# Kernel tuning notes

Measured on AMD Instinct MI355X. Metric: run time of the kernel, lower is better.

## Reference

```python
import jax, jax.numpy as jnp
import numpy as np

T, D, H, C, MAXLEN = 1024, 512, 512, 50257, 150


def setup_inputs() -> dict:
    key = jax.random.key(0)
    ks = iter(jax.random.split(key, 32))
    s = 0.1  # keep gates out of saturation
    def p(shape):
        return jax.random.normal(next(ks), shape, jnp.float32) * s
    return {
        "x": jax.random.normal(next(ks), (T, D), jnp.float32),
        "enc_Wih0": p((2, 4 * H, D)), "enc_Whh0": p((2, 4 * H, H)), "enc_b0": p((2, 4 * H)),
        "enc_Wih1": p((2, 4 * H, 2 * H)), "enc_Whh1": p((2, 4 * H, H)), "enc_b1": p((2, 4 * H)),
        "dec_Wih0": p((2, 4 * H, D)), "dec_Whh0": p((2, 4 * H, H)), "dec_b0": p((2, 4 * H)),
        "dec_Wih1": p((2, 4 * H, 2 * H)), "dec_Whh1": p((2, 4 * H, H)), "dec_b1": p((2, 4 * H)),
        "lin_W": p((C, 2 * H)), "lin_b": p((C,)),
        "emb": p((C, D)),
        "bos": p((D,)),
        "out_max_len": MAXLEN,
    }


def _cell(x, h, c, Wih, Whh, b):
    # PyTorch LSTM gate order: i, f, g, o; b = b_ih + b_hh
    g = Wih @ x + Whh @ h + b
    i, f, gg, o = jnp.split(g, 4)
    c = jax.nn.sigmoid(f) * c + jax.nn.sigmoid(i) * jnp.tanh(gg)
    h = jax.nn.sigmoid(o) * jnp.tanh(c)
    return h, c


def _run_dir(xs, Wih, Whh, b, reverse):
    Hh = Whh.shape[1]
    init = (jnp.zeros((Hh,), xs.dtype), jnp.zeros((Hh,), xs.dtype))
    def step(carry, xt):
        h, c = carry
        h, c = _cell(xt, h, c, Wih, Whh, b)
        return (h, c), h
    (hT, cT), hs = jax.lax.scan(step, init, xs, reverse=reverse)
    return hs, hT, cT  # hs aligned with input order


def _encode(x, layers):
    xs = x  # [T, D]
    h_fin, c_fin = [], []
    for (Wih, Whh, b) in layers:
        hs_f, hf, cf = _run_dir(xs, Wih[0], Whh[0], b[0], False)
        hs_b, hb, cb = _run_dir(xs, Wih[1], Whh[1], b[1], True)
        xs = jnp.concatenate([hs_f, hs_b], axis=-1)  # [T, 2H]
        h_fin.append(jnp.stack([hf, hb]))
        c_fin.append(jnp.stack([cf, cb]))
    return jnp.stack(h_fin), jnp.stack(c_fin)  # [L, 2, H]


def reference(x, enc_Wih0, enc_Whh0, enc_b0, enc_Wih1, enc_Whh1, enc_b1,
              dec_Wih0, dec_Whh0, dec_b0, dec_Wih1, dec_Whh1, dec_b1,
              lin_W, lin_b, emb, bos, out_max_len):
    layers_enc = [(enc_Wih0, enc_Whh0, enc_b0), (enc_Wih1, enc_Whh1, enc_b1)]
    layers_dec = [(dec_Wih0, dec_Whh0, dec_b0), (dec_Wih1, dec_Whh1, dec_b1)]

    h, c = _encode(x, layers_enc)  # [2, 2, H] each

    def dec_step(carry, _):
        buf, h, c = carry
        inp = buf
        nh, nc = [], []
        for l, (Wih, Whh, b) in enumerate(layers_dec):
            hf, cf = _cell(inp, h[l, 0], c[l, 0], Wih[0], Whh[0], b[0])
            hb, cb = _cell(inp, h[l, 1], c[l, 1], Wih[1], Whh[1], b[1])
            inp = jnp.concatenate([hf, hb])  # [2H]
            nh.append(jnp.stack([hf, hb]))
            nc.append(jnp.stack([cf, cb]))
        logits = lin_W @ inp + lin_b          # [C]
        tok = jnp.argmax(logits)              # greedy feedback
        buf = emb[tok]                        # [D]
        return (buf, jnp.stack(nh), jnp.stack(nc)), (logits, tok)

    _, (logits_seq, toks) = jax.lax.scan(dec_step, (bos, h, c), None, length=out_max_len)
    return logits_seq, toks  # [L_out, C], [L_out]
```

## Files before the change

### kernel.cpp

```cpp
#include <hip/hip_runtime.h>
#include <hip/hip_fp16.h>

typedef unsigned int u32;
typedef unsigned short u16;
typedef unsigned long long u64;

#define DEV static __device__ __forceinline__

DEV float sigf(float x){ return 1.0f / (1.0f + expf(-x)); }

DEV u64  ldA64(const u64* p){ return __hip_atomic_load(p, __ATOMIC_RELAXED, __HIP_MEMORY_SCOPE_AGENT); }
DEV void stA64(u64* p, u64 v){ __hip_atomic_store(p, v, __ATOMIC_RELAXED, __HIP_MEMORY_SCOPE_AGENT); }
DEV float ldAf(const float* p){ return __hip_atomic_load(p, __ATOMIC_RELAXED, __HIP_MEMORY_SCOPE_AGENT); }
DEV void stAf(float* p, float v){ __hip_atomic_store(p, v, __ATOMIC_RELAXED, __HIP_MEMORY_SCOPE_AGENT); }
DEV u32  ldA32(const u32* p){ return __hip_atomic_load(p, __ATOMIC_RELAXED, __HIP_MEMORY_SCOPE_AGENT); }

DEV u64 packHV(float h, u32 tag){ return (((u64)__float_as_uint(h)) << 32) | (u64)tag; }
DEV float unpackH(u64 v){ return __uint_as_float((u32)(v >> 32)); }

DEV u64 packKeyT(float v, u32 row, u32 tagv){
  u32 u = __float_as_uint(v);
  u = (u & 0x80000000u) ? ~u : (u | 0x80000000u);
  return (((u64)u) << 32) | ((u64)(0x1FFFFu - row) << 15) | (u64)tagv;
}

DEV float dot8h(const uint4 A, const float4 a, const float4 b){
  const __half2* h = (const __half2*)&A;
  const float2 f0 = __half22float2(h[0]);
  const float2 f1 = __half22float2(h[1]);
  const float2 f2 = __half22float2(h[2]);
  const float2 f3 = __half22float2(h[3]);
  float s;
  s  = f0.x*a.x + f0.y*a.y + f1.x*a.z + f1.y*a.w;
  s += f2.x*b.x + f2.y*b.y + f3.x*b.z + f3.y*b.w;
  return s;
}

DEV float dotrow(const float4 A, const float4 B, const float4 Cc, const float4 D,
                 const float4 q0, const float4 q1, const float4 q2, const float4 q3){
  float s;
  s  = A.x*q0.x + A.y*q0.y + A.z*q0.z + A.w*q0.w;
  s += B.x*q1.x + B.y*q1.y + B.z*q1.z + B.w*q1.w;
  s += Cc.x*q2.x + Cc.y*q2.y + Cc.z*q2.z + Cc.w*q2.w;
  s += D.x*q3.x + D.y*q3.y + D.z*q3.z + D.w*q3.w;
  return s;
}

struct SM {
  float w1s[24576];
  float inpP[1600];
  float linp[1024];
  float h0c[1024];
  float srow[200];
  float erow[200];
  float red[8];
  float dots[16];
  float cst0[4];
  float cst1[4];
  u64   wkey[4];
};

template<int CPT> DEV int pidx(int c){ int b = c / CPT; return b * (CPT + 4) + (c - b * CPT); }

template<int CPT, int DIN>
DEV void loadw(float* wreg, const float* Wih, const float* Whh, int jb4){
  const int tid = threadIdx.x, r = tid >> 4, p = tid & 15;
  const int R = 512 * (r >> 2) + jb4 + (r & 3);
  const float* s1 = Wih + (size_t)R * DIN;
  const float* s2 = Whh + (size_t)R * 512;
  #pragma unroll
  for (int k = 0; k < CPT; k += 4){
    const int col = p * CPT + k;
    const float4 v = *(const float4*)((col < DIN) ? (s1 + col) : (s2 + col - DIN));
    wreg[k] = v.x; wreg[k+1] = v.y; wreg[k+2] = v.z; wreg[k+3] = v.w;
  }
}

template<int CPT>
DEV void dot16(const float* wreg, const float* inpP, float* dots){
  const int tid = threadIdx.x, p = tid & 15;
  const float* xi = inpP + p * (CPT + 4);
  float acc = 0.f;
  #pragma unroll
  for (int k = 0; k < CPT; k += 4){
    const float4 xv = *(const float4*)(xi + k);
    acc = fmaf(wreg[k],   xv.x, acc);
    acc = fmaf(wreg[k+1], xv.y, acc);
    acc = fmaf(wreg[k+2], xv.z, acc);
    acc = fmaf(wreg[k+3], xv.w, acc);
  }
  #pragma unroll
  for (int s = 1; s < 16; s <<= 1) acc += __shfl_xor(acc, s, 64);
  if (p == 0) dots[tid >> 4] = acc;
}

DEV void dot16_w1(const float* w1s, const float* inpP, float* dots){
  const int tid = threadIdx.x, p = tid & 15;
  const float* xi = inpP + p * 100;
  float acc = 0.f;
  #pragma unroll
  for (int k = 0; k < 96; k += 4){
    const float4 w4 = *(const float4*)(w1s + (k >> 2) * 1024 + tid * 4);
    const float4 xv = *(const float4*)(xi + k);
    acc = fmaf(w4.x, xv.x, acc);
    acc = fmaf(w4.y, xv.y, acc);
    acc = fmaf(w4.z, xv.z, acc);
    acc = fmaf(w4.w, xv.w, acc);
  }
  #pragma unroll
  for (int s = 1; s < 16; s <<= 1) acc += __shfl_xor(acc, s, 64);
  if (p == 0) dots[tid >> 4] = acc;
}

DEV void gbar_phase(u32* g, u32 ev){
  __syncthreads();
  if (threadIdx.x == 0){
    __hip_atomic_fetch_add(g, 1u, __ATOMIC_RELEASE, __HIP_MEMORY_SCOPE_AGENT);
    const u32 tgt = 256u * ev;
    while (ldA32(g) < tgt) __builtin_amdgcn_s_sleep(8);
    (void)__hip_atomic_fetch_add(g, 0u, __ATOMIC_ACQUIRE, __HIP_MEMORY_SCOPE_AGENT);
    asm volatile("" ::: "memory");
  }
  __syncthreads();
}

template<int DIN, bool WRITE_XS>
DEV void enc_layer(const float* __restrict__ xg, float* __restrict__ xs_out,
                   const float* __restrict__ Wih, const float* __restrict__ Whh,
                   const float* __restrict__ bias,
                   u64* __restrict__ ht, float* __restrict__ hfinL, float* __restrict__ cfinL,
                   const int dir, const int jb4, SM& sm)
{
  constexpr int CPT = (DIN + 512) / 16;
  constexpr int NX  = DIN / 256;
  const int tid = threadIdx.x;
  float wreg[CPT];
  loadw<CPT, DIN>(wreg, Wih + (size_t)dir * 2048 * DIN, Whh + (size_t)dir * 2048 * 512, jb4);
  float b_i = 0.f, b_f = 0.f, b_g = 0.f, b_o = 0.f;
  if (tid < 4){
    const int j = jb4 + tid;
    sm.cst0[tid] = 0.f;
    b_i = bias[dir*2048 +        j];
    b_f = bias[dir*2048 +  512 + j];
    b_g = bias[dir*2048 + 1024 + j];
    b_o = bias[dir*2048 + 1536 + j];
  }
  float xr[NX];
  {
    const int t0 = dir ? 1023 : 0;
    #pragma unroll
    for (int i = 0; i < NX; ++i){
      const int c = tid + 256 * i;
      xr[i] = (DIN == 512) ? xg[(size_t)t0 * DIN + c] : ldAf(xg + (size_t)t0 * DIN + c);
    }
  }
  for (int step = 0; step < 1024; ++step){
    #pragma unroll
    for (int i = 0; i < NX; ++i) sm.inpP[pidx<CPT>(tid + 256 * i)] = xr[i];
    {
      const u64* hp = ht + (step & 1) * 512;
      const u32 want = (u32)step;
      u64 a = ldA64(hp + tid*2), b = ldA64(hp + tid*2 + 1);
      while ((u32)a != want){ __builtin_amdgcn_s_sleep(1); a = ldA64(hp + tid*2); }
      while ((u32)b != want){ __builtin_amdgcn_s_sleep(1); b = ldA64(hp + tid*2 + 1); }
      sm.inpP[pidx<CPT>(DIN + tid*2)]     = unpackH(a);
      sm.inpP[pidx<CPT>(DIN + tid*2 + 1)] = unpackH(b);
    }
    __syncthreads();
    if (step < 1023){
      const int tn = dir ? (1022 - step) : (step + 1);
      #pragma unroll
      for (int i = 0; i < NX; ++i){
        const int c = tid + 256 * i;
        xr[i] = (DIN == 512) ? xg[(size_t)tn * DIN + c] : ldAf(xg + (size_t)tn * DIN + c);
      }
    }
    dot16<CPT>(wreg, sm.inpP, sm.dots);
    __syncthreads();
    if (tid < 4){
      const float gi = sm.dots[tid]      + b_i;
      const float gf = sm.dots[4 + tid]  + b_f;
      const float gg = sm.dots[8 + tid]  + b_g;
      const float go = sm.dots[12 + tid] + b_o;
      const float cc = sigf(gf) * sm.cst0[tid] + sigf(gi) * tanhf(gg);
      const float hh = sigf(go) * tanhf(cc);
      sm.cst0[tid] = cc;
      const int t = dir ? (1023 - step) : step;
      const int j = jb4 + tid;
      stA64(ht + ((step + 1) & 1) * 512 + j, packHV(hh, (u32)(step + 1)));
      if (WRITE_XS) stAf(xs_out + (size_t)t * 1024 + dir * 512 + j, hh);
      if (step == 1023){ stAf(hfinL + dir*512 + j, hh); stAf(cfinL + dir*512 + j, cc); }
    }
    __syncthreads();
  }
}

__global__ void bilstm_init(u32* ws){
  for (u32 i = threadIdx.x; i < 32768u; i += 256u) ws[i] = 0u;
}

__global__ void cvt_lin(const float* __restrict__ w, uint4* __restrict__ o,
                        float* __restrict__ maxw, const int C){
  const int wv = threadIdx.x >> 6, lane = threadIdx.x & 63;
  const int stride = gridDim.x * 4;
  for (int r = blockIdx.x * 4 + wv; r < C; r += stride){
    const float4* src = (const float4*)(w + (size_t)r * 1024) + lane * 4;
    const float4 v0 = src[0], v1 = src[1], v2 = src[2], v3 = src[3];
    uint4 p0, p1;
    __half2 h;
    h = __floats2half2_rn(v0.x, v0.y); p0.x = *(const u32*)&h;
    h = __floats2half2_rn(v0.z, v0.w); p0.y = *(const u32*)&h;
    h = __floats2half2_rn(v1.x, v1.y); p0.z = *(const u32*)&h;
    h = __floats2half2_rn(v1.z, v1.w); p0.w = *(const u32*)&h;
    h = __floats2half2_rn(v2.x, v2.y); p1.x = *(const u32*)&h;
    h = __floats2half2_rn(v2.z, v2.w); p1.y = *(const u32*)&h;
    h = __floats2half2_rn(v3.x, v3.y); p1.z = *(const u32*)&h;
    h = __floats2half2_rn(v3.z, v3.w); p1.w = *(const u32*)&h;
    uint4* dst = o + (size_t)r * 128 + lane * 2;
    dst[0] = p0; dst[1] = p1;
    float m = fmaxf(fmaxf(fmaxf(fabsf(v0.x), fabsf(v0.y)), fmaxf(fabsf(v0.z), fabsf(v0.w))),
                    fmaxf(fmaxf(fabsf(v1.x), fabsf(v1.y)), fmaxf(fabsf(v1.z), fabsf(v1.w))));
    m = fmaxf(m, fmaxf(fmaxf(fabsf(v2.x), fabsf(v2.y)), fmaxf(fabsf(v2.z), fabsf(v2.w))));
    m = fmaxf(m, fmaxf(fmaxf(fabsf(v3.x), fabsf(v3.y)), fmaxf(fabsf(v3.z), fabsf(v3.w))));
    #pragma unroll
    for (int s = 1; s < 64; s <<= 1) m = fmaxf(m, __shfl_xor(m, s, 64));
    if (lane == 0) maxw[r] = m;
  }
}

template<int LINFP16>
__global__ __launch_bounds__(256, 1)
void bilstm_persist(const float* __restrict__ x,
                    const float* __restrict__ eW0, const float* __restrict__ eU0, const float* __restrict__ eb0,
                    const float* __restrict__ eW1, const float* __restrict__ eU1, const float* __restrict__ eb1,
                    const float* __restrict__ dW0, const float* __restrict__ dU0, const float* __restrict__ db0,
                    const float* __restrict__ dW1, const float* __restrict__ dU1, const float* __restrict__ db1,
                    const float* __restrict__ linW, const float* __restrict__ linb,
                    const float* __restrict__ emb, const float* __restrict__ bos,
                    float* __restrict__ out, float* __restrict__ ws, const int L, const int C)
{
  __shared__ SM sm;
  const int w = blockIdx.x;
  const int tid = threadIdx.x;
  const int dir = (w >> 2) & 1;
  const int jb4 = ((w >> 3) * 4 + (w & 3)) * 4;

  u64*  htagE = (u64*)ws;
  u64*  h0t   = htagE + 4096;
  u64*  h1t   = h0t + 2048;
  float* hfin = (float*)(h1t + 2048);
  float* cfin = hfin + 2048;
  u32*  gbar  = (u32*)(cfin + 2048);
  u64*  gkey  = (u64*)((char*)ws + 98304);
  const u16*  linH = (const u16*)((const char*)ws + 131072);
  const float* maxw = (const float*)((const char*)ws + 131072 + (size_t)C * 2048);
  float* xs1  = out;

  enc_layer<512,  true >(x,   xs1,     eW0, eU0, eb0, htagE + (0*2 + dir)*1024, hfin,        cfin,        dir, jb4, sm);
  gbar_phase(gbar, 1);
  enc_layer<1024, false>(xs1, nullptr, eW1, eU1, eb1, htagE + (1*2 + dir)*1024, hfin + 1024, cfin + 1024, dir, jb4, sm);
  gbar_phase(gbar, 2);

  float w0reg[64];
  loadw<64, 512>(w0reg, dW0 + (size_t)dir*2048*512, dU0 + (size_t)dir*2048*512, jb4);
  {
    const int r = tid >> 4, p = tid & 15;
    const int R = 512 * (r >> 2) + jb4 + (r & 3);
    const float* s1 = dW1 + (size_t)dir*2048*1024 + (size_t)R * 1024;
    const float* s2 = dU1 + (size_t)dir*2048*512  + (size_t)R * 512;
    #pragma unroll
    for (int k = 0; k < 96; k += 4){
      const int col = p * 96 + k;
      const float4 v = *(const float4*)((col < 1024) ? (s1 + col) : (s2 + col - 1024));
      *(float4*)(sm.w1s + (k >> 2) * 1024 + tid * 4) = v;
    }
  }

  float b0i=0,b0f=0,b0g=0,b0o=0, b1i=0,b1f=0,b1g=0,b1o=0;
  if (tid < 4){
    const int j = jb4 + tid;
    sm.cst0[tid] = ldAf(&cfin[dir*512 + j]);
    sm.cst1[tid] = ldAf(&cfin[1024 + dir*512 + j]);
    b0i = db0[dir*2048 + j];        b0f = db0[dir*2048 + 512 + j];
    b0g = db0[dir*2048 + 1024 + j]; b0o = db0[dir*2048 + 1536 + j];
    b1i = db1[dir*2048 + j];        b1f = db1[dir*2048 + 512 + j];
    b1g = db1[dir*2048 + 1024 + j]; b1o = db1[dir*2048 + 1536 + j];
  }
  const int rbase = w * 196 + (w < 81 ? w : 81);
  const int rn    = 196 + (w < 81 ? 1 : 0);
  int tok = 0;

  for (int t = 0; t < L; ++t){
    const u32 tag = (u32)(t + 1);
    {
      const float* src = (t == 0) ? bos : (emb + (size_t)tok * 512);
      sm.inpP[pidx<64>(tid)]       = src[tid];
      sm.inpP[pidx<64>(tid + 256)] = src[tid + 256];
      if (t == 0){
        sm.inpP[pidx<64>(512 + tid*2)]     = ldAf(&hfin[dir*512 + tid*2]);
        sm.inpP[pidx<64>(512 + tid*2 + 1)] = ldAf(&hfin[dir*512 + tid*2 + 1]);
      } else {
        sm.inpP[pidx<64>(512 + tid*2)]     = sm.h0c[dir*512 + tid*2];
        sm.inpP[pidx<64>(512 + tid*2 + 1)] = sm.h0c[dir*512 + tid*2 + 1];
      }
      __syncthreads();
      dot16<64>(w0reg, sm.inpP, sm.dots);
      __syncthreads();
      if (tid < 4){
        const float gi = sm.dots[tid] + b0i, gf = sm.dots[4+tid] + b0f;
        const float gg = sm.dots[8+tid] + b0g, go = sm.dots[12+tid] + b0o;
        const float cc = sigf(gf) * sm.cst0[tid] + sigf(gi) * tanhf(gg);
        const float hh = sigf(go) * tanhf(cc);
        sm.cst0[tid] = cc;
        stA64(h0t + (dir*2 + (t & 1))*512 + jb4 + tid, packHV(hh, tag));
      }
      __syncthreads();
    }

    {
      #pragma unroll
      for (int i = 0; i < 4; ++i){
        const int c = tid + 256 * i;
        const int d = c >> 9, idx = c & 511;
        const u64* hp = h0t + (d*2 + (t & 1)) * 512 + idx;
        u64 v = ldA64(hp);
        while ((u32)v != tag){ __builtin_amdgcn_s_sleep(1); v = ldA64(hp); }
        const float hv = unpackH(v);
        sm.inpP[pidx<96>(c)] = hv;
        sm.h0c[c] = hv;
      }
      if (t == 0){
        sm.inpP[pidx<96>(1024 + tid*2)]     = ldAf(&hfin[1024 + dir*512 + tid*2]);
        sm.inpP[pidx<96>(1024 + tid*2 + 1)] = ldAf(&hfin[1024 + dir*512 + tid*2 + 1]);
      } else {
        sm.inpP[pidx<96>(1024 + tid*2)]     = sm.linp[dir*512 + tid*2];
        sm.inpP[pidx<96>(1024 + tid*2 + 1)] = sm.linp[dir*512 + tid*2 + 1];
      }
      __syncthreads();
      dot16_w1(sm.w1s, sm.inpP, sm.dots);
      __syncthreads();
      if (tid < 4){
        const float gi = sm.dots[tid] + b1i, gf = sm.dots[4+tid] + b1f;
        const float gg = sm.dots[8+tid] + b1g, go = sm.dots[12+tid] + b1o;
        const float cc = sigf(gf) * sm.cst1[tid] + sigf(gi) * tanhf(gg);
        const float hh = sigf(go) * tanhf(cc);
        sm.cst1[tid] = cc;
        stA64(h1t + (dir*2 + (t & 1))*512 + jb4 + tid, packHV(hh, tag));
      }
    }

    {
      float pabs = 0.f;
      #pragma unroll
      for (int i = 0; i < 4; ++i){
        const int c = tid + 256 * i;
        const int d = c >> 9, idx = c & 511;
        const u64* hp = h1t + (d*2 + (t & 1)) * 512 + idx;
        u64 v = ldA64(hp);
        while ((u32)v != tag){ __builtin_amdgcn_s_sleep(1); v = ldA64(hp); }
        const float hv = unpackH(v);
        sm.linp[c] = hv;
        pabs += fabsf(hv);
      }
      const int wv = tid >> 6, lane = tid & 63;
      if constexpr (LINFP16){
        #pragma unroll
        for (int s = 1; s < 64; s <<= 1) pabs += __shfl_xor(pabs, s, 64);
        if (lane == 0) sm.red[wv] = pabs;
      }
      __syncthreads();

      const float4* ip4 = (const float4*)(sm.linp + lane * 16);
      const float4 q0 = ip4[0], q1 = ip4[1], q2 = ip4[2], q3 = ip4[3];
      u64 kmax = 0;
      const int rmaxr = rbase + rn - 1;

      if constexpr (LINFP16){
        const float sumabs = sm.red[0] + sm.red[1] + sm.red[2] + sm.red[3];
        const float cErr = sumabs * 7.5e-4f;
        float lb = -1e30f;
        for (int i0 = wv; i0 < rn; i0 += 16){
          const int ia = i0;
          const int ib = (i0 + 4  > rn - 1) ? rn - 1 : i0 + 4;
          const int ic = (i0 + 8  > rn - 1) ? rn - 1 : i0 + 8;
          const int id = (i0 + 12 > rn - 1) ? rn - 1 : i0 + 12;
          const int ra = rbase + ia, rb = rbase + ib, rc = rbase + ic, rd = rbase + id;
          const uint4* pa = (const uint4*)(linH + (size_t)ra * 1024) + lane * 2;
          const uint4* pb = (const uint4*)(linH + (size_t)rb * 1024) + lane * 2;
          const uint4* pc = (const uint4*)(linH + (size_t)rc * 1024) + lane * 2;
          const uint4* pd = (const uint4*)(linH + (size_t)rd * 1024) + lane * 2;
          const uint4 A0 = pa[0], A1 = pa[1];
          const uint4 B0 = pb[0], B1 = pb[1];
          const uint4 C0 = pc[0], C1 = pc[1];
          const uint4 D0 = pd[0], D1 = pd[1];
          float sa = dot8h(A0, q0, q1) + dot8h(A1, q2, q3);
          float sb = dot8h(B0, q0, q1) + dot8h(B1, q2, q3);
          float sc = dot8h(C0, q0, q1) + dot8h(C1, q2, q3);
          float sd = dot8h(D0, q0, q1) + dot8h(D1, q2, q3);
          #pragma unroll
          for (int sh = 1; sh < 64; sh <<= 1){
            sa += __shfl_xor(sa, sh, 64);
            sb += __shfl_xor(sb, sh, 64);
            sc += __shfl_xor(sc, sh, 64);
            sd += __shfl_xor(sd, sh, 64);
          }
          if (lane == 0){
            sa += linb[ra]; sb += linb[rb]; sc += linb[rc]; sd += linb[rd];
            out[(size_t)t * C + ra] = sa;
            out[(size_t)t * C + rb] = sb;
            out[(size_t)t * C + rc] = sc;
            out[(size_t)t * C + rd] = sd;
            const float ea = maxw[ra] * cErr + 1e-4f;
            const float eb = maxw[rb] * cErr + 1e-4f;
            const float ec = maxw[rc] * cErr + 1e-4f;
            const float ed = maxw[rd] * cErr + 1e-4f;
            sm.srow[ia] = sa; sm.erow[ia] = ea;
            sm.srow[ib] = sb; sm.erow[ib] = eb;
            sm.srow[ic] = sc; sm.erow[ic] = ec;
            sm.srow[id] = sd; sm.erow[id] = ed;
            lb = fmaxf(lb, sa - ea); lb = fmaxf(lb, sb - eb);
            lb = fmaxf(lb, sc - ec); lb = fmaxf(lb, sd - ed);
          }
        }
        if (lane == 0) sm.red[4 + wv] = lb;
        __syncthreads();
        const float Lb = fmaxf(fmaxf(sm.red[4], sm.red[5]), fmaxf(sm.red[6], sm.red[7]));
        for (int i = wv; i < rn; i += 4){
          if (sm.srow[i] + sm.erow[i] >= Lb){
            const int row = rbase + i;
            const float4* wp = (const float4*)(linW + (size_t)row * 1024) + lane * 4;
            float s = dotrow(wp[0], wp[1], wp[2], wp[3], q0, q1, q2, q3);
            #pragma unroll
            for (int sh2 = 1; sh2 < 64; sh2 <<= 1) s += __shfl_xor(s, sh2, 64);
            if (lane == 0){
              s += linb[row];
              const u64 k = packKeyT(s, (u32)row, tag);
              if (k > kmax) kmax = k;
            }
          }
        }
      } else {
        for (int i0 = wv; i0 < rn; i0 += 16){
          const int ra = rbase + i0;
          const int rb = (ra + 4  > rmaxr) ? rmaxr : ra + 4;
          const int rc = (ra + 8  > rmaxr) ? rmaxr : ra + 8;
          const int rd = (ra + 12 > rmaxr) ? rmaxr : ra + 12;
          const float ba = linb[ra], bb = linb[rb], bc = linb[rc], bd = linb[rd];
          const float4* pa = (const float4*)(linW + (size_t)ra * 1024) + lane * 4;
          const float4* pb = (const float4*)(linW + (size_t)rb * 1024) + lane * 4;
          const float4* pc = (const float4*)(linW + (size_t)rc * 1024) + lane * 4;
          const float4* pd = (const float4*)(linW + (size_t)rd * 1024) + lane * 4;
          const float4 a0 = pa[0], a1 = pa[1], a2 = pa[2], a3 = pa[3];
          const float4 e0 = pb[0], e1 = pb[1], e2 = pb[2], e3 = pb[3];
          const float4 c0 = pc[0], c1 = pc[1], c2 = pc[2], c3 = pc[3];
          const float4 d0 = pd[0], d1 = pd[1], d2 = pd[2], d3 = pd[3];
          float sa = dotrow(a0,a1,a2,a3, q0,q1,q2,q3);
          float sb = dotrow(e0,e1,e2,e3, q0,q1,q2,q3);
          float sc = dotrow(c0,c1,c2,c3, q0,q1,q2,q3);
          float sd = dotrow(d0,d1,d2,d3, q0,q1,q2,q3);
          #pragma unroll
          for (int sh = 1; sh < 64; sh <<= 1){
            sa += __shfl_xor(sa, sh, 64);
            sb += __shfl_xor(sb, sh, 64);
            sc += __shfl_xor(sc, sh, 64);
            sd += __shfl_xor(sd, sh, 64);
          }
          if (lane == 0){
            sa += ba; sb += bb; sc += bc; sd += bd;
            out[(size_t)t * C + ra] = sa;
            out[(size_t)t * C + rb] = sb;
            out[(size_t)t * C + rc] = sc;
            out[(size_t)t * C + rd] = sd;
            u64 k;
            k = packKeyT(sa, (u32)ra, tag); if (k > kmax) kmax = k;
            k = packKeyT(sb, (u32)rb, tag); if (k > kmax) kmax = k;
            k = packKeyT(sc, (u32)rc, tag); if (k > kmax) kmax = k;
            k = packKeyT(sd, (u32)rd, tag); if (k > kmax) kmax = k;
          }
        }
      }
      if (lane == 0) sm.wkey[wv] = kmax;
    }

    __syncthreads();
    if (tid == 0){
      u64 k4 = sm.wkey[0];
      if (sm.wkey[1] > k4) k4 = sm.wkey[1];
      if (sm.wkey[2] > k4) k4 = sm.wkey[2];
      if (sm.wkey[3] > k4) k4 = sm.wkey[3];
      stA64(gkey + (size_t)w * 16, k4);
    }
    __syncthreads();
    {
      const u64* p = gkey + (size_t)tid * 16;
      u64 kv = ldA64(p);
      while ((u32)(kv & 0x7FFFu) != tag){ __builtin_amdgcn_s_sleep(1); kv = ldA64(p); }
      #pragma unroll
      for (int s = 1; s < 64; s <<= 1){
        const u64 o = (u64)__shfl_xor((unsigned long long)kv, s, 64);
        if (o > kv) kv = o;
      }
      if ((tid & 63) == 0) sm.wkey[tid >> 6] = kv;
    }
    __syncthreads();
    {
      u64 gk = sm.wkey[0];
      if (sm.wkey[1] > gk) gk = sm.wkey[1];
      if (sm.wkey[2] > gk) gk = sm.wkey[2];
      if (sm.wkey[3] > gk) gk = sm.wkey[3];
      tok = (int)(0x1FFFFu - ((u32)(gk >> 15) & 0x1FFFFu));
      if (w == 0 && tid == 0) out[(size_t)L * C + t] = (float)tok;
    }
  }
}

extern "C" void kernel_launch(void* const* d_in, const int* in_sizes, int n_in,
                              void* d_out, int out_size, void* d_ws, size_t ws_size,
                              hipStream_t stream)
{
  const float* x    = (const float*)d_in[0];
  const float* eW0  = (const float*)d_in[1];
  const float* eU0  = (const float*)d_in[2];
  const float* eb0  = (const float*)d_in[3];
  const float* eW1  = (const float*)d_in[4];
  const float* eU1  = (const float*)d_in[5];
  const float* eb1  = (const float*)d_in[6];
  const float* dW0  = (const float*)d_in[7];
  const float* dU0  = (const float*)d_in[8];
  const float* db0  = (const float*)d_in[9];
  const float* dW1  = (const float*)d_in[10];
  const float* dU1  = (const float*)d_in[11];
  const float* db1  = (const float*)d_in[12];
  const float* linW = (const float*)d_in[13];
  const float* linb = (const float*)d_in[14];
  const float* emb  = (const float*)d_in[15];
  const float* bos  = (const float*)d_in[16];

  const int C = in_sizes[14];
  const int L = out_size / (C + 1);
  const int nlin = in_sizes[13];

  const size_t need = 131072 + (size_t)nlin * 2 + (size_t)C * 4;
  const bool fp16lin = (ws_size >= need);

  hipLaunchKernelGGL(bilstm_init, dim3(1), dim3(256), 0, stream, (u32*)d_ws);
  if (fp16lin){
    hipLaunchKernelGGL(cvt_lin, dim3(2048), dim3(256), 0, stream,
                       linW, (uint4*)((char*)d_ws + 131072),
                       (float*)((char*)d_ws + 131072 + (size_t)C * 2048), C);
    hipLaunchKernelGGL((bilstm_persist<1>), dim3(256), dim3(256), 0, stream,
                       x, eW0, eU0, eb0, eW1, eU1, eb1,
                       dW0, dU0, db0, dW1, dU1, db1,
                       linW, linb, emb, bos,
                       (float*)d_out, (float*)d_ws, L, C);
  } else {
    hipLaunchKernelGGL((bilstm_persist<0>), dim3(256), dim3(256), 0, stream,
                       x, eW0, eU0, eb0, eW1, eU1, eb1,
                       dW0, dU0, db0, dW1, dU1, db1,
                       linW, linb, emb, bos,
                       (float*)d_out, (float*)d_ws, L, C);
  }
}
```

Measured before the change: 8.815 ms.

## Double block size to 512 threads, using extra waves for the vocab projection

Launches the persistent kernel with 512 threads per block. Only the first 256 threads take part in the recurrent LSTM steps, while all 8 waves share the vocabulary projection and argmax rows, with row stride and reduction arrays widened to match. This is meant to hide more memory latency in the bandwidth-bound linear/argmax phase. In exchange, the register budget per thread is halved under launch_bounds(512,1), which may spill the register-resident weights (64+ floats per thread) and add barrier cost to the latency-critical recurrent steps.

```diff
diff --git a/kernel.cpp b/kernel.cpp
--- a/kernel.cpp
+++ b/kernel.cpp
@@ -53,11 +53,11 @@
   float h0c[1024];
   float srow[200];
   float erow[200];
-  float red[8];
+  float red[16];
   float dots[16];
   float cst0[4];
   float cst1[4];
-  u64   wkey[4];
+  u64   wkey[8];
 };
 
 template<int CPT> DEV int pidx(int c){ int b = c / CPT; return b * (CPT + 4) + (c - b * CPT); }
@@ -134,8 +134,10 @@
   constexpr int CPT = (DIN + 512) / 16;
   constexpr int NX  = DIN / 256;
   const int tid = threadIdx.x;
+  const bool act = tid < 256;
   float wreg[CPT];
-  loadw<CPT, DIN>(wreg, Wih + (size_t)dir * 2048 * DIN, Whh + (size_t)dir * 2048 * 512, jb4);
+  if (act)
+    loadw<CPT, DIN>(wreg, Wih + (size_t)dir * 2048 * DIN, Whh + (size_t)dir * 2048 * 512, jb4);
   float b_i = 0.f, b_f = 0.f, b_g = 0.f, b_o = 0.f;
   if (tid < 4){
     const int j = jb4 + tid;
@@ -146,7 +148,7 @@
     b_o = bias[dir*2048 + 1536 + j];
   }
   float xr[NX];
-  {
+  if (act){
     const int t0 = dir ? 1023 : 0;
     #pragma unroll
     for (int i = 0; i < NX; ++i){
@@ -155,9 +157,9 @@
     }
   }
   for (int step = 0; step < 1024; ++step){
-    #pragma unroll
-    for (int i = 0; i < NX; ++i) sm.inpP[pidx<CPT>(tid + 256 * i)] = xr[i];
-    {
+    if (act){
+      #pragma unroll
+      for (int i = 0; i < NX; ++i) sm.inpP[pidx<CPT>(tid + 256 * i)] = xr[i];
       const u64* hp = ht + (step & 1) * 512;
       const u32 want = (u32)step;
       u64 a = ldA64(hp + tid*2), b = ldA64(hp + tid*2 + 1);
@@ -167,15 +169,17 @@
       sm.inpP[pidx<CPT>(DIN + tid*2 + 1)] = unpackH(b);
     }
     __syncthreads();
-    if (step < 1023){
-      const int tn = dir ? (1022 - step) : (step + 1);
-      #pragma unroll
-      for (int i = 0; i < NX; ++i){
-        const int c = tid + 256 * i;
-        xr[i] = (DIN == 512) ? xg[(size_t)tn * DIN + c] : ldAf(xg + (size_t)tn * DIN + c);
-      }
-    }
-    dot16<CPT>(wreg, sm.inpP, sm.dots);
+    if (act){
+      if (step < 1023){
+        const int tn = dir ? (1022 - step) : (step + 1);
+        #pragma unroll
+        for (int i = 0; i < NX; ++i){
+          const int c = tid + 256 * i;
+          xr[i] = (DIN == 512) ? xg[(size_t)tn * DIN + c] : ldAf(xg + (size_t)tn * DIN + c);
+        }
+      }
+      dot16<CPT>(wreg, sm.inpP, sm.dots);
+    }
     __syncthreads();
     if (tid < 4){
       const float gi = sm.dots[tid]      + b_i;
@@ -229,7 +233,7 @@
 }
 
 template<int LINFP16>
-__global__ __launch_bounds__(256, 1)
+__global__ __launch_bounds__(512, 1)
 void bilstm_persist(const float* __restrict__ x,
                     const float* __restrict__ eW0, const float* __restrict__ eU0, const float* __restrict__ eb0,
                     const float* __restrict__ eW1, const float* __restrict__ eU1, const float* __restrict__ eb1,
@@ -242,6 +246,7 @@
   __shared__ SM sm;
   const int w = blockIdx.x;
   const int tid = threadIdx.x;
+  const bool act = tid < 256;
   const int dir = (w >> 2) & 1;
   const int jb4 = ((w >> 3) * 4 + (w & 3)) * 4;
 
@@ -262,8 +267,9 @@
   gbar_phase(gbar, 2);
 
   float w0reg[64];
-  loadw<64, 512>(w0reg, dW0 + (size_t)dir*2048*512, dU0 + (size_t)dir*2048*512, jb4);
-  {
+  if (act)
+    loadw<64, 512>(w0reg, dW0 + (size_t)dir*2048*512, dU0 + (size_t)dir*2048*512, jb4);
+  if (act){
     const int r = tid >> 4, p = tid & 15;
     const int R = 512 * (r >> 2) + jb4 + (r & 3);
     const float* s1 = dW1 + (size_t)dir*2048*1024 + (size_t)R * 1024;
@@ -293,18 +299,20 @@
   for (int t = 0; t < L; ++t){
     const u32 tag = (u32)(t + 1);
     {
-      const float* src = (t == 0) ? bos : (emb + (size_t)tok * 512);
-      sm.inpP[pidx<64>(tid)]       = src[tid];
-      sm.inpP[pidx<64>(tid + 256)] = src[tid + 256];
-      if (t == 0){
-        sm.inpP[pidx<64>(512 + tid*2)]     = ldAf(&hfin[dir*512 + tid*2]);
-        sm.inpP[pidx<64>(512 + tid*2 + 1)] = ldAf(&hfin[dir*512 + tid*2 + 1]);
-      } else {
-        sm.inpP[pidx<64>(512 + tid*2)]     = sm.h0c[dir*512 + tid*2];
-        sm.inpP[pidx<64>(512 + tid*2 + 1)] = sm.h0c[dir*512 + tid*2 + 1];
+      if (act){
+        const float* src = (t == 0) ? bos : (emb + (size_t)tok * 512);
+        sm.inpP[pidx<64>(tid)]       = src[tid];
+        sm.inpP[pidx<64>(tid + 256)] = src[tid + 256];
+        if (t == 0){
+          sm.inpP[pidx<64>(512 + tid*2)]     = ldAf(&hfin[dir*512 + tid*2]);
+          sm.inpP[pidx<64>(512 + tid*2 + 1)] = ldAf(&hfin[dir*512 + tid*2 + 1]);
+        } else {
+          sm.inpP[pidx<64>(512 + tid*2)]     = sm.h0c[dir*512 + tid*2];
+          sm.inpP[pidx<64>(512 + tid*2 + 1)] = sm.h0c[dir*512 + tid*2 + 1];
+        }
       }
       __syncthreads();
-      dot16<64>(w0reg, sm.inpP, sm.dots);
+      if (act) dot16<64>(w0reg, sm.inpP, sm.dots);
       __syncthreads();
       if (tid < 4){
         const float gi = sm.dots[tid] + b0i, gf = sm.dots[4+tid] + b0f;
@@ -318,26 +326,28 @@
     }
 
     {
-      #pragma unroll
-      for (int i = 0; i < 4; ++i){
-        const int c = tid + 256 * i;
-        const int d = c >> 9, idx = c & 511;
-        const u64* hp = h0t + (d*2 + (t & 1)) * 512 + idx;
-        u64 v = ldA64(hp);
-        while ((u32)v != tag){ __builtin_amdgcn_s_sleep(1); v = ldA64(hp); }
-        const float hv = unpackH(v);
-        sm.inpP[pidx<96>(c)] = hv;
-        sm.h0c[c] = hv;
-      }
-      if (t == 0){
-        sm.inpP[pidx<96>(1024 + tid*2)]     = ldAf(&hfin[1024 + dir*512 + tid*2]);
-        sm.inpP[pidx<96>(1024 + tid*2 + 1)] = ldAf(&hfin[1024 + dir*512 + tid*2 + 1]);
-      } else {
-        sm.inpP[pidx<96>(1024 + tid*2)]     = sm.linp[dir*512 + tid*2];
-        sm.inpP[pidx<96>(1024 + tid*2 + 1)] = sm.linp[dir*512 + tid*2 + 1];
+      if (act){
+        #pragma unroll
+        for (int i = 0; i < 4; ++i){
+          const int c = tid + 256 * i;
+          const int d = c >> 9, idx = c & 511;
+          const u64* hp = h0t + (d*2 + (t & 1)) * 512 + idx;
+          u64 v = ldA64(hp);
+          while ((u32)v != tag){ __builtin_amdgcn_s_sleep(1); v = ldA64(hp); }
+          const float hv = unpackH(v);
+          sm.inpP[pidx<96>(c)] = hv;
+          sm.h0c[c] = hv;
+        }
+        if (t == 0){
+          sm.inpP[pidx<96>(1024 + tid*2)]     = ldAf(&hfin[1024 + dir*512 + tid*2]);
+          sm.inpP[pidx<96>(1024 + tid*2 + 1)] = ldAf(&hfin[1024 + dir*512 + tid*2 + 1]);
+        } else {
+          sm.inpP[pidx<96>(1024 + tid*2)]     = sm.linp[dir*512 + tid*2];
+          sm.inpP[pidx<96>(1024 + tid*2 + 1)] = sm.linp[dir*512 + tid*2 + 1];
+        }
       }
       __syncthreads();
-      dot16_w1(sm.w1s, sm.inpP, sm.dots);
+      if (act) dot16_w1(sm.w1s, sm.inpP, sm.dots);
       __syncthreads();
       if (tid < 4){
         const float gi = sm.dots[tid] + b1i, gf = sm.dots[4+tid] + b1f;
@@ -350,23 +360,25 @@
     }
 
     {
-      float pabs = 0.f;
-      #pragma unroll
-      for (int i = 0; i < 4; ++i){
-        const int c = tid + 256 * i;
-        const int d = c >> 9, idx = c & 511;
-        const u64* hp = h1t + (d*2 + (t & 1)) * 512 + idx;
-        u64 v = ldA64(hp);
-        while ((u32)v != tag){ __builtin_amdgcn_s_sleep(1); v = ldA64(hp); }
-        const float hv = unpackH(v);
-        sm.linp[c] = hv;
-        pabs += fabsf(hv);
-      }
       const int wv = tid >> 6, lane = tid & 63;
-      if constexpr (LINFP16){
+      if (act){
+        float pabs = 0.f;
         #pragma unroll
-        for (int s = 1; s < 64; s <<= 1) pabs += __shfl_xor(pabs, s, 64);
-        if (lane == 0) sm.red[wv] = pabs;
+        for (int i = 0; i < 4; ++i){
+          const int c = tid + 256 * i;
+          const int d = c >> 9, idx = c & 511;
+          const u64* hp = h1t + (d*2 + (t & 1)) * 512 + idx;
+          u64 v = ldA64(hp);
+          while ((u32)v != tag){ __builtin_amdgcn_s_sleep(1); v = ldA64(hp); }
+          const float hv = unpackH(v);
+          sm.linp[c] = hv;
+          pabs += fabsf(hv);
+        }
+        if constexpr (LINFP16){
+          #pragma unroll
+          for (int s = 1; s < 64; s <<= 1) pabs += __shfl_xor(pabs, s, 64);
+          if (lane == 0) sm.red[wv] = pabs;
+        }
       }
       __syncthreads();
 
@@ -379,11 +391,11 @@
         const float sumabs = sm.red[0] + sm.red[1] + sm.red[2] + sm.red[3];
         const float cErr = sumabs * 7.5e-4f;
         float lb = -1e30f;
-        for (int i0 = wv; i0 < rn; i0 += 16){
+        for (int i0 = wv; i0 < rn; i0 += 32){
           const int ia = i0;
-          const int ib = (i0 + 4  > rn - 1) ? rn - 1 : i0 + 4;
-          const int ic = (i0 + 8  > rn - 1) ? rn - 1 : i0 + 8;
-          const int id = (i0 + 12 > rn - 1) ? rn - 1 : i0 + 12;
+          const int ib = (i0 + 8  > rn - 1) ? rn - 1 : i0 + 8;
+          const int ic = (i0 + 16 > rn - 1) ? rn - 1 : i0 + 16;
+          const int id = (i0 + 24 > rn - 1) ? rn - 1 : i0 + 24;
           const int ra = rbase + ia, rb = rbase + ib, rc = rbase + ic, rd = rbase + id;
           const uint4* pa = (const uint4*)(linH + (size_t)ra * 1024) + lane * 2;
           const uint4* pb = (const uint4*)(linH + (size_t)rb * 1024) + lane * 2;
@@ -422,10 +434,12 @@
             lb = fmaxf(lb, sc - ec); lb = fmaxf(lb, sd - ed);
           }
         }
-        if (lane == 0) sm.red[4 + wv] = lb;
+        if (lane == 0) sm.red[8 + wv] = lb;
         __syncthreads();
-        const float Lb = fmaxf(fmaxf(sm.red[4], sm.red[5]), fmaxf(sm.red[6], sm.red[7]));
-        for (int i = wv; i < rn; i += 4){
+        float Lb = sm.red[8];
+        #pragma unroll
+        for (int i = 9; i < 16; ++i) Lb = fmaxf(Lb, sm.red[i]);
+        for (int i = wv; i < rn; i += 8){
           if (sm.srow[i] + sm.erow[i] >= Lb){
             const int row = rbase + i;
             const float4* wp = (const float4*)(linW + (size_t)row * 1024) + lane * 4;
@@ -440,11 +454,11 @@
           }
         }
       } else {
-        for (int i0 = wv; i0 < rn; i0 += 16){
+        for (int i0 = wv; i0 < rn; i0 += 32){
           const int ra = rbase + i0;
-          const int rb = (ra + 4  > rmaxr) ? rmaxr : ra + 4;
-          const int rc = (ra + 8  > rmaxr) ? rmaxr : ra + 8;
-          const int rd = (ra + 12 > rmaxr) ? rmaxr : ra + 12;
+          const int rb = (rbase + i0 + 8  > rmaxr) ? rmaxr : rbase + i0 + 8;
+          const int rc = (rbase + i0 + 16 > rmaxr) ? rmaxr : rbase + i0 + 16;
+          const int rd = (rbase + i0 + 24 > rmaxr) ? rmaxr : rbase + i0 + 24;
           const float ba = linb[ra], bb = linb[rb], bc = linb[rc], bd = linb[rd];
           const float4* pa = (const float4*)(linW + (size_t)ra * 1024) + lane * 4;
           const float4* pb = (const float4*)(linW + (size_t)rb * 1024) + lane * 4;
@@ -485,13 +499,12 @@
     __syncthreads();
     if (tid == 0){
       u64 k4 = sm.wkey[0];
-      if (sm.wkey[1] > k4) k4 = sm.wkey[1];
-      if (sm.wkey[2] > k4) k4 = sm.wkey[2];
-      if (sm.wkey[3] > k4) k4 = sm.wkey[3];
+      #pragma unroll
+      for (int i = 1; i < 8; ++i) if (sm.wkey[i] > k4) k4 = sm.wkey[i];
       stA64(gkey + (size_t)w * 16, k4);
     }
     __syncthreads();
-    {
+    if (act){
       const u64* p = gkey + (size_t)tid * 16;
       u64 kv = ldA64(p);
       while ((u32)(kv & 0x7FFFu) != tag){ __builtin_amdgcn_s_sleep(1); kv = ldA64(p); }
@@ -548,13 +561,13 @@
     hipLaunchKernelGGL(cvt_lin, dim3(2048), dim3(256), 0, stream,
                        linW, (uint4*)((char*)d_ws + 131072),
                        (float*)((char*)d_ws + 131072 + (size_t)C * 2048), C);
-    hipLaunchKernelGGL((bilstm_persist<1>), dim3(256), dim3(256), 0, stream,
+    hipLaunchKernelGGL((bilstm_persist<1>), dim3(256), dim3(512), 0, stream,
                        x, eW0, eU0, eb0, eW1, eU1, eb1,
                        dW0, dU0, db0, dW1, dU1, db1,
                        linW, linb, emb, bos,
                        (float*)d_out, (float*)d_ws, L, C);
   } else {
-    hipLaunchKernelGGL((bilstm_persist<0>), dim3(256), dim3(256), 0, stream,
+    hipLaunchKernelGGL((bilstm_persist<0>), dim3(256), dim3(512), 0, stream,
                        x, eW0, eU0, eb0, eW1, eU1, eb1,
                        dW0, dU0, db0, dW1, dU1, db1,
                        linW, linb, emb, bos,
```

Result: faster. 8.317 ms (-5.6%).
